# Optimization experiments

Measured on AMD Instinct MI355X. Metric: run time of the kernel, lower is better.

The kernel has to match this reference:

```python
import jax, jax.numpy as jnp
import numpy as np

NEG = -1e30  # log-space 'minus infinity' that stays finite in fp32 arithmetic
BLANK = 0


def _lse3(a, b, c):
    m = jnp.maximum(jnp.maximum(a, b), c)
    return m + jnp.log(jnp.exp(a - m) + jnp.exp(b - m) + jnp.exp(c - m))


def setup_inputs() -> dict:
    key = jax.random.key(0)
    k1, k2, k3, k4 = jax.random.split(key, 4)
    B, T, C, L = 16, 512, 4096, 128
    scores = jax.random.normal(k1, (B, T, C), dtype=jnp.float32)
    labels = jax.random.randint(k2, (B, L), 1, C, dtype=jnp.int64)      # no blanks in targets
    feat_lens = jax.random.randint(k3, (B,), 384, T + 1, dtype=jnp.int64)
    label_lens = jax.random.randint(k4, (B,), 64, L + 1, dtype=jnp.int64)
    return {"scores": scores, "labels": labels, "feat_lens": feat_lens, "label_lens": label_lens}


def reference(scores, labels, feat_lens, label_lens):
    # scores: [B, T, C]. Matches torch: log_softmax then nn.CTCLoss(blank=0,
    # reduction='mean', zero_infinity=True).
    scores = scores.astype(jnp.float32)
    log_probs = jax.nn.log_softmax(scores, axis=-1)                      # [B, T, C]
    B, T, C = scores.shape
    L = labels.shape[1]
    S = 2 * L + 1  # extended label: blank, l1, blank, ..., lL, blank

    ext = jnp.full((B, S), BLANK, dtype=labels.dtype).at[:, 1::2].set(labels)
    # Gather per-(t, extended-symbol) log-probs once: [B, T, S]
    lp = jnp.take_along_axis(log_probs, jnp.broadcast_to(ext[:, None, :], (B, T, S)), axis=2)

    # skip transition s-2 -> s allowed iff ext[s] != blank and ext[s] != ext[s-2]
    skip = jnp.concatenate(
        [jnp.zeros((B, 2), bool), (ext[:, 2:] != ext[:, :-2]) & (ext[:, 2:] != BLANK)], axis=1)

    alpha0 = jnp.full((B, S), NEG, dtype=jnp.float32).at[:, 0].set(lp[:, 0, 0])
    alpha0 = alpha0.at[:, 1].set(jnp.where(label_lens > 0, lp[:, 0, 1], NEG))

    lp_t_first = jnp.swapaxes(lp, 0, 1)  # [T, B, S]

    def step(alpha, xs):
        lp_t, t = xs
        a1 = jnp.pad(alpha, ((0, 0), (1, 0)), constant_values=NEG)[:, :S]
        a2 = jnp.pad(alpha, ((0, 0), (2, 0)), constant_values=NEG)[:, :S]
        a2 = jnp.where(skip, a2, NEG)
        new = lp_t + _lse3(alpha, a1, a2)
        alpha = jnp.where((t < feat_lens)[:, None], new, alpha)  # freeze past feat_len
        return alpha, None

    alpha, _ = jax.lax.scan(step, alpha0, (lp_t_first[1:], jnp.arange(1, T)))

    end = 2 * label_lens  # index of final blank per sample
    a_end = jnp.take_along_axis(alpha, end[:, None], axis=1)[:, 0]
    a_end1 = jnp.where(
        label_lens > 0,
        jnp.take_along_axis(alpha, jnp.maximum(end - 1, 0)[:, None], axis=1)[:, 0], NEG)
    m = jnp.maximum(a_end, a_end1)
    log_lik = m + jnp.log(jnp.exp(a_end - m) + jnp.exp(a_end1 - m))
    loss = -log_lik
    loss = jnp.where(loss > 0.5e30, 0.0, loss)  # zero_infinity=True
    denom = jnp.maximum(label_lens, 1).astype(loss.dtype)
    return jnp.mean(loss / denom)  # torch 'mean': divide by target_lengths, then batch mean
```

## Files before the change

### kernel.cpp

```cpp
#include <hip/hip_runtime.h>

#define T_ 512
#define C_ 4096
#define L_ 128
#define RCPLN2 1.4426950408889634f
#define LN2 0.6931471805599453f
#define NEGL (-1e30f)
#define SCALE_CTR 4.722366482869645e21f
#define SCALE_LOG 72.0f

__device__ __forceinline__ float fexp2(float x) { return __builtin_amdgcn_exp2f(x); }
__device__ __forceinline__ float flog2(float x) { return __builtin_amdgcn_logf(x); }
__device__ __forceinline__ float frcp(float x)  { return __builtin_amdgcn_rcpf(x); }
__device__ __forceinline__ float lg(float x)    { return (x > 0.f) ? flog2(x) : NEGL; }

__global__ __launch_bounds__(256) void k_lse_gather(
    const float* __restrict__ scores, const int* __restrict__ labels,
    const int* __restrict__ feat_lens,
    float* __restrict__ p_lab, float* __restrict__ p_blank) {
  const int row = blockIdx.x;
  const int b = row >> 9;
  const int t = row & (T_ - 1);
  if (t >= feat_lens[b]) return;

  __shared__ float sRow[C_];
  __shared__ float sSum[4];
  const float4* __restrict__ rp4 = (const float4*)(scores + (size_t)row * C_);
  float4* sRow4 = (float4*)sRow;
  const int tid = threadIdx.x;

  float s0 = 0.f, s1 = 0.f, s2 = 0.f, s3 = 0.f;
#pragma unroll
  for (int k = 0; k < 4; ++k) {
    float4 v = rp4[tid + 256 * k];
    sRow4[tid + 256 * k] = v;
    s0 += fexp2(v.x * RCPLN2);
    s1 += fexp2(v.y * RCPLN2);
    s2 += fexp2(v.z * RCPLN2);
    s3 += fexp2(v.w * RCPLN2);
  }
  float s = (s0 + s1) + (s2 + s3);
#pragma unroll
  for (int off = 32; off; off >>= 1) s += __shfl_down(s, off);
  const int wid = tid >> 6, lane = tid & 63;
  if (lane == 0) sSum[wid] = s;
  __syncthreads();
  const float l2sum = flog2((sSum[0] + sSum[1]) + (sSum[2] + sSum[3]));

  if (tid < L_) {
    const int lab = labels[b * L_ + tid];
    p_lab[(size_t)row * L_ + tid] = fexp2(sRow[lab] * RCPLN2 - l2sum);
  } else if (tid == L_) {
    p_blank[row] = fexp2(sRow[0] * RCPLN2 - l2sum);
  }
}

__global__ __launch_bounds__(128) void k_ctc_dp(
    const float* __restrict__ p_lab, const float* __restrict__ p_blank,
    const int* __restrict__ labels, const int* __restrict__ feat_lens,
    const int* __restrict__ label_lens, float* __restrict__ loss_out) {
  const int b = blockIdx.x;
  const int lane = threadIdx.x & 63;
  const int wid = threadIdx.x >> 6;
  const int flen = feat_lens[b];
  const int llen = label_lens[b];
  const int tm = flen >> 1;

  const int l0 = labels[b * L_ + 2 * lane];
  const int l1 = labels[b * L_ + 2 * lane + 1];
  const int lm1 = __shfl_up(l1, 1);
  const int ln0 = __shfl_down(l0, 1);
  const bool skip1 = (lane > 0) && (l0 != lm1);
  const bool skip3 = (l1 != l0);
  const bool skipd = (lane < 63) && (ln0 != l1);

  const float2* __restrict__ llp = (const float2*)(p_lab + (size_t)b * T_ * L_);
  const float* __restrict__ lpl = p_lab + (size_t)b * T_ * L_;
  const float* __restrict__ lbp = p_blank + b * T_;

  __shared__ float sB[257];
  __shared__ float sSb;

  if (wid == 0) {
    const float2 ll0 = llp[lane];
    float a0 = (lane == 0) ? lbp[0] : 0.f;
    float a1 = (lane == 0) ? ll0.x : 0.f;
    float a2 = 0.f, a3 = 0.f, a4 = 0.f;
    float p = 0.f;
    float Sa = 0.f;

    float2 cc[4]; float cb[4];
#pragma unroll
    for (int k = 0; k < 4; ++k) {
      const int tt = min(1 + k, flen - 1);
      cc[k] = llp[tt * 64 + lane]; cb[k] = lbp[tt];
    }
    int t = 1;
    while (t <= tm) {
      float2 nc[4]; float nb[4];
#pragma unroll
      for (int k = 0; k < 4; ++k) {
        const int tt = min(t + 4 + k, flen - 1);
        nc[k] = llp[tt * 64 + lane]; nb[k] = lbp[tt];
      }
#pragma unroll
      for (int k = 0; k < 4; ++k) {
        if (t + k <= tm) {
          const float n3 = cc[k].y * (a3 + a2 + (skip3 ? a1 : 0.f));
          const float n4 = cb[k] * (a4 + a3);
          const float pn = __shfl_up(n3, 1);
          const float n0 = cb[k] * (a0 + p);
          const float n1 = cc[k].x * (a1 + a0 + (skip1 ? p : 0.f));
          const float n2 = cb[k] * (a2 + a1);
          a0 = n0; a1 = n1; a2 = n2; a3 = n3;
          a4 = (lane == 63) ? n4 : 0.f;
          p = (lane == 0) ? 0.f : pn;
        }
        if (k & 1) {
          float m = fmaxf(fmaxf(fmaxf(a0, a1), fmaxf(a2, a3)), a4);
#pragma unroll
          for (int off = 1; off < 64; off <<= 1) m = fmaxf(m, __shfl_xor(m, off));
          const float r = frcp(m) * SCALE_CTR;
          Sa += flog2(m) - SCALE_LOG;
          a0 *= r; a1 *= r; a2 *= r; a3 *= r; a4 *= r; p *= r;
        }
      }
#pragma unroll
      for (int k = 0; k < 4; ++k) { cc[k] = nc[k]; cb[k] = nb[k]; }
      t += 4;
    }
    const float2 cce = llp[tm * 64 + lane];
    const float cbe = lbp[tm];
    const float lb2 = flog2(cbe), lc0 = flog2(cce.x), lc1 = flog2(cce.y);
    const float la0 = lg(a0), la1 = lg(a1), la2 = lg(a2), la3 = lg(a3);
    const float la4 = lg(a4);
    __syncthreads();
    float w0 = la0 + sB[4 * lane + 0] - lb2;
    float w1 = la1 + sB[4 * lane + 1] - lc0;
    float w2 = la2 + sB[4 * lane + 2] - lb2;
    float w3 = la3 + sB[4 * lane + 3] - lc1;
    float m = fmaxf(fmaxf(w0, w1), fmaxf(w2, w3));
    float w4 = NEGL;
    if (lane == 63) { w4 = la4 + sB[256] - lb2; m = fmaxf(m, w4); }
#pragma unroll
    for (int off = 1; off < 64; off <<= 1) m = fmaxf(m, __shfl_xor(m, off));
    float sum = fexp2(w0 - m) + fexp2(w1 - m) + fexp2(w2 - m) + fexp2(w3 - m);
    if (lane == 63) sum += fexp2(w4 - m);
#pragma unroll
    for (int off = 1; off < 64; off <<= 1) sum += __shfl_xor(sum, off);
    if (lane == 0) {
      const float l2lik = m + flog2(sum) + Sa + sSb;
      float loss = -LN2 * l2lik;
      if (loss > 0.5e30f || !(loss == loss)) loss = 0.0f;
      loss_out[b] = loss / (float)llen;
    }
  } else {
    const int e = 2 * llen;
    const float ve = lbp[flen - 1];
    const float vo = lpl[(size_t)(flen - 1) * L_ + (llen - 1)];
    float b0 = (4 * lane == e) ? ve : 0.f;
    float b1 = (4 * lane + 1 == e - 1) ? vo : 0.f;
    float b2 = (4 * lane + 2 == e) ? ve : 0.f;
    float b3 = (4 * lane + 3 == e - 1) ? vo : 0.f;
    float b4 = (lane == 63 && e == 256) ? ve : 0.f;
    float q0 = __shfl_down(b0, 1); q0 = (lane == 63) ? b4 : q0;
    float q1 = __shfl_down(b1, 1); q1 = (lane == 63) ? 0.f : q1;
    float Sb = 0.f;

    float2 cc[4]; float cb[4];
    int t = flen - 2;
#pragma unroll
    for (int k = 0; k < 4; ++k) {
      const int tt = max(t - k, tm);
      cc[k] = llp[tt * 64 + lane]; cb[k] = lbp[tt];
    }
    while (t >= tm) {
      float2 nc[4]; float nb[4];
#pragma unroll
      for (int k = 0; k < 4; ++k) {
        const int tt = max(t - 4 - k, tm);
        nc[k] = llp[tt * 64 + lane]; nb[k] = lbp[tt];
      }
#pragma unroll
      for (int k = 0; k < 4; ++k) {
        if (t - k >= tm) {
          const float n0 = cb[k] * (b0 + b1);
          const float n1 = cc[k].x * (b1 + b2 + (skip3 ? b3 : 0.f));
          const float n4 = cb[k] * b4;
          const float q0n = __shfl_down(n0, 1);
          const float q1n = __shfl_down(n1, 1);
          const float n3 = cc[k].y * (b3 + q0 + (skipd ? q1 : 0.f));
          const float n2 = cb[k] * (b2 + b3);
          b0 = n0; b1 = n1; b2 = n2; b3 = n3; b4 = n4;
          q0 = (lane == 63) ? n4 : q0n;
          q1 = (lane == 63) ? 0.f : q1n;
        }
        if (k & 1) {
          float m = fmaxf(fmaxf(fmaxf(b0, b1), fmaxf(b2, b3)), b4);
#pragma unroll
          for (int off = 1; off < 64; off <<= 1) m = fmaxf(m, __shfl_xor(m, off));
          const float r = frcp(m) * SCALE_CTR;
          Sb += flog2(m) - SCALE_LOG;
          b0 *= r; b1 *= r; b2 *= r; b3 *= r; b4 *= r; q0 *= r; q1 *= r;
        }
      }
#pragma unroll
      for (int k = 0; k < 4; ++k) { cc[k] = nc[k]; cb[k] = nb[k]; }
      t -= 4;
    }
    sB[4 * lane + 0] = lg(b0);
    sB[4 * lane + 1] = lg(b1);
    sB[4 * lane + 2] = lg(b2);
    sB[4 * lane + 3] = lg(b3);
    if (lane == 63) sB[256] = lg(b4);
    if (lane == 0) sSb = Sb;
    __syncthreads();
  }
}

__global__ __launch_bounds__(64) void k_final(const float* __restrict__ loss_out,
                                              float* __restrict__ out, int B) {
  const int tid = threadIdx.x;
  float v = (tid < B) ? loss_out[tid] : 0.0f;
#pragma unroll
  for (int off = 32; off; off >>= 1) v += __shfl_down(v, off);
  if (tid == 0) out[0] = v / (float)B;
}

extern "C" void kernel_launch(void* const* d_in, const int* in_sizes, int n_in,
                              void* d_out, int out_size, void* d_ws, size_t ws_size,
                              hipStream_t stream) {
  const float* scores = (const float*)d_in[0];
  const int* labels = (const int*)d_in[1];
  const int* feat_lens = (const int*)d_in[2];
  const int* label_lens = (const int*)d_in[3];
  const int B = in_sizes[2];

  float* p_lab = (float*)d_ws;
  float* p_blank = p_lab + (size_t)B * T_ * L_;
  float* loss_out = p_blank + (size_t)B * T_;
  float* out = (float*)d_out;

  k_lse_gather<<<B * T_, 256, 0, stream>>>(scores, labels, feat_lens, p_lab, p_blank);
  k_ctc_dp<<<B, 128, 0, stream>>>(p_lab, p_blank, labels, feat_lens, label_lens, loss_out);
  k_final<<<1, 64, 0, stream>>>(loss_out, out, B);
}
```

Before: 243.7 us.

## Use DPP lane shifts and reductions in CTC DP, deepen prefetch

Replaces __shfl_up/__shfl_down/__shfl_xor (LDS-permute based) in the forward and backward CTC recurrences with DPP row/wave shift instructions and a DPP-based wave max reduction. The per-step latency of the serial DP chain is meant to drop. Prefetch depth is doubled to two groups of four timesteps ahead, and the forward loop's midpoint is rounded down to a multiple of four so the per-step bounds check can be removed. The wave_shr/shl DPP controls with bound_ctrl supply zero at the boundary lanes, which replaces the explicit lane-0/lane-63 selects. The approach depends on the DPP wave-shift controls being supported on this architecture.

```diff
diff --git a/kernel.cpp b/kernel.cpp
--- a/kernel.cpp
+++ b/kernel.cpp
@@ -13,6 +13,27 @@
 __device__ __forceinline__ float flog2(float x) { return __builtin_amdgcn_logf(x); }
 __device__ __forceinline__ float frcp(float x)  { return __builtin_amdgcn_rcpf(x); }
 __device__ __forceinline__ float lg(float x)    { return (x > 0.f) ? flog2(x) : NEGL; }
+
+template <int CTRL>
+__device__ __forceinline__ float dppmov(float v) {
+  return __int_as_float(__builtin_amdgcn_update_dpp(
+      0, __float_as_int(v), CTRL, 0xF, 0xF, true));
+}
+__device__ __forceinline__ float wshr1(float v) { return dppmov<0x138>(v); }
+__device__ __forceinline__ float wshl1(float v) { return dppmov<0x130>(v); }
+template <int CTRL>
+__device__ __forceinline__ float maxdpp(float v) {
+  return fmaxf(v, dppmov<CTRL>(v));
+}
+__device__ __forceinline__ float wavemax(float v) {
+  v = maxdpp<0xB1>(v);
+  v = maxdpp<0x4E>(v);
+  v = maxdpp<0x141>(v);
+  v = maxdpp<0x140>(v);
+  v = maxdpp<0x142>(v);
+  v = maxdpp<0x143>(v);
+  return __int_as_float(__builtin_amdgcn_readlane(__float_as_int(v), 63));
+}
 
 __global__ __launch_bounds__(256) void k_lse_gather(
     const float* __restrict__ scores, const int* __restrict__ labels,
@@ -64,7 +85,7 @@
   const int wid = threadIdx.x >> 6;
   const int flen = feat_lens[b];
   const int llen = label_lens[b];
-  const int tm = flen >> 1;
+  const int tm = (flen >> 1) & ~3;
 
   const int l0 = labels[b * L_ + 2 * lane];
   const int l1 = labels[b * L_ + 2 * lane + 1];
@@ -89,44 +110,45 @@
     float p = 0.f;
     float Sa = 0.f;
 
-    float2 cc[4]; float cb[4];
-#pragma unroll
-    for (int k = 0; k < 4; ++k) {
-      const int tt = min(1 + k, flen - 1);
-      cc[k] = llp[tt * 64 + lane]; cb[k] = lbp[tt];
+    float2 cc[4], nc[4]; float cb[4], nb[4];
+#pragma unroll
+    for (int k = 0; k < 4; ++k) {
+      cc[k] = llp[(1 + k) * 64 + lane]; cb[k] = lbp[1 + k];
+    }
+#pragma unroll
+    for (int k = 0; k < 4; ++k) {
+      const int tt = min(5 + k, flen - 1);
+      nc[k] = llp[tt * 64 + lane]; nb[k] = lbp[tt];
     }
     int t = 1;
     while (t <= tm) {
-      float2 nc[4]; float nb[4];
-#pragma unroll
-      for (int k = 0; k < 4; ++k) {
-        const int tt = min(t + 4 + k, flen - 1);
-        nc[k] = llp[tt * 64 + lane]; nb[k] = lbp[tt];
-      }
-#pragma unroll
-      for (int k = 0; k < 4; ++k) {
-        if (t + k <= tm) {
-          const float n3 = cc[k].y * (a3 + a2 + (skip3 ? a1 : 0.f));
-          const float n4 = cb[k] * (a4 + a3);
-          const float pn = __shfl_up(n3, 1);
-          const float n0 = cb[k] * (a0 + p);
-          const float n1 = cc[k].x * (a1 + a0 + (skip1 ? p : 0.f));
-          const float n2 = cb[k] * (a2 + a1);
-          a0 = n0; a1 = n1; a2 = n2; a3 = n3;
-          a4 = (lane == 63) ? n4 : 0.f;
-          p = (lane == 0) ? 0.f : pn;
-        }
+      float2 mc[4]; float mb[4];
+#pragma unroll
+      for (int k = 0; k < 4; ++k) {
+        const int tt = min(t + 8 + k, flen - 1);
+        mc[k] = llp[tt * 64 + lane]; mb[k] = lbp[tt];
+      }
+#pragma unroll
+      for (int k = 0; k < 4; ++k) {
+        const float n3 = cc[k].y * (a3 + a2 + (skip3 ? a1 : 0.f));
+        const float n4 = cb[k] * (a4 + a3);
+        const float pn = wshr1(n3);
+        const float n0 = cb[k] * (a0 + p);
+        const float n1 = cc[k].x * (a1 + a0 + (skip1 ? p : 0.f));
+        const float n2 = cb[k] * (a2 + a1);
+        a0 = n0; a1 = n1; a2 = n2; a3 = n3;
+        a4 = (lane == 63) ? n4 : 0.f;
+        p = pn;
         if (k & 1) {
-          float m = fmaxf(fmaxf(fmaxf(a0, a1), fmaxf(a2, a3)), a4);
-#pragma unroll
-          for (int off = 1; off < 64; off <<= 1) m = fmaxf(m, __shfl_xor(m, off));
+          const float m = wavemax(fmaxf(fmaxf(fmaxf(a0, a1), fmaxf(a2, a3)), a4));
           const float r = frcp(m) * SCALE_CTR;
           Sa += flog2(m) - SCALE_LOG;
           a0 *= r; a1 *= r; a2 *= r; a3 *= r; a4 *= r; p *= r;
         }
       }
 #pragma unroll
-      for (int k = 0; k < 4; ++k) { cc[k] = nc[k]; cb[k] = nb[k]; }
+      for (int k = 0; k < 4; ++k) { cc[k] = nc[k]; cb[k] = nb[k];
+                                    nc[k] = mc[k]; nb[k] = mb[k]; }
       t += 4;
     }
     const float2 cce = llp[tm * 64 + lane];
@@ -167,19 +189,24 @@
     float q1 = __shfl_down(b1, 1); q1 = (lane == 63) ? 0.f : q1;
     float Sb = 0.f;
 
-    float2 cc[4]; float cb[4];
+    float2 cc[4], nc[4]; float cb[4], nb[4];
     int t = flen - 2;
 #pragma unroll
     for (int k = 0; k < 4; ++k) {
       const int tt = max(t - k, tm);
       cc[k] = llp[tt * 64 + lane]; cb[k] = lbp[tt];
     }
+#pragma unroll
+    for (int k = 0; k < 4; ++k) {
+      const int tt = max(t - 4 - k, tm);
+      nc[k] = llp[tt * 64 + lane]; nb[k] = lbp[tt];
+    }
     while (t >= tm) {
-      float2 nc[4]; float nb[4];
-#pragma unroll
-      for (int k = 0; k < 4; ++k) {
-        const int tt = max(t - 4 - k, tm);
-        nc[k] = llp[tt * 64 + lane]; nb[k] = lbp[tt];
+      float2 mc[4]; float mb[4];
+#pragma unroll
+      for (int k = 0; k < 4; ++k) {
+        const int tt = max(t - 8 - k, tm);
+        mc[k] = llp[tt * 64 + lane]; mb[k] = lbp[tt];
       }
 #pragma unroll
       for (int k = 0; k < 4; ++k) {
@@ -187,25 +214,24 @@
           const float n0 = cb[k] * (b0 + b1);
           const float n1 = cc[k].x * (b1 + b2 + (skip3 ? b3 : 0.f));
           const float n4 = cb[k] * b4;
-          const float q0n = __shfl_down(n0, 1);
-          const float q1n = __shfl_down(n1, 1);
+          const float q0n = wshl1(n0);
+          const float q1n = wshl1(n1);
           const float n3 = cc[k].y * (b3 + q0 + (skipd ? q1 : 0.f));
           const float n2 = cb[k] * (b2 + b3);
           b0 = n0; b1 = n1; b2 = n2; b3 = n3; b4 = n4;
           q0 = (lane == 63) ? n4 : q0n;
-          q1 = (lane == 63) ? 0.f : q1n;
+          q1 = q1n;
         }
         if (k & 1) {
-          float m = fmaxf(fmaxf(fmaxf(b0, b1), fmaxf(b2, b3)), b4);
-#pragma unroll
-          for (int off = 1; off < 64; off <<= 1) m = fmaxf(m, __shfl_xor(m, off));
+          const float m = wavemax(fmaxf(fmaxf(fmaxf(b0, b1), fmaxf(b2, b3)), b4));
           const float r = frcp(m) * SCALE_CTR;
           Sb += flog2(m) - SCALE_LOG;
           b0 *= r; b1 *= r; b2 *= r; b3 *= r; b4 *= r; q0 *= r; q1 *= r;
         }
       }
 #pragma unroll
-      for (int k = 0; k < 4; ++k) { cc[k] = nc[k]; cb[k] = nb[k]; }
+      for (int k = 0; k < 4; ++k) { cc[k] = nc[k]; cb[k] = nb[k];
+                                    nc[k] = mc[k]; nb[k] = mb[k]; }
       t -= 4;
     }
     sB[4 * lane + 0] = lg(b0);
```

Result: faster. 222.1 us (-8.9%).

## Speed up CTC DP with DPP shifts, exponent rescaling, deeper prefetch, fused final reduce

Applied to the files above, without the earlier changes.

Lane shifts and the wave max reduction in the alpha/beta recurrences now use DPP row/wave moves instead of ds_bpermute shuffles. Rescaling now works by adjusting the float exponent and keeps an integer scale count, which removes the rcp and log from the serial critical path. Label probabilities are prefetched in four rotating 8-step buffers rather than 4-step ones, and the midpoint is rounded to an even step. The separate final kernel is replaced by an atomic counter where the last block computes the mean, at the cost of an extra memset launch and atomics.

```diff
diff --git a/kernel.cpp b/kernel.cpp
--- a/kernel.cpp
+++ b/kernel.cpp
@@ -6,13 +6,25 @@
 #define RCPLN2 1.4426950408889634f
 #define LN2 0.6931471805599453f
 #define NEGL (-1e30f)
-#define SCALE_CTR 4.722366482869645e21f
-#define SCALE_LOG 72.0f
 
 __device__ __forceinline__ float fexp2(float x) { return __builtin_amdgcn_exp2f(x); }
 __device__ __forceinline__ float flog2(float x) { return __builtin_amdgcn_logf(x); }
-__device__ __forceinline__ float frcp(float x)  { return __builtin_amdgcn_rcpf(x); }
 __device__ __forceinline__ float lg(float x)    { return (x > 0.f) ? flog2(x) : NEGL; }
+
+template <int CTRL>
+__device__ __forceinline__ float dppmov(float v) {
+  return __int_as_float(__builtin_amdgcn_update_dpp(
+      0, __float_as_int(v), CTRL, 0xF, 0xF, true));
+}
+__device__ __forceinline__ float wshr1(float v) { return dppmov<0x138>(v); }
+__device__ __forceinline__ float wshl1(float v) { return dppmov<0x130>(v); }
+template <int CTRL>
+__device__ __forceinline__ float maxdpp(float v) { return fmaxf(v, dppmov<CTRL>(v)); }
+__device__ __forceinline__ float wavemax(float v) {
+  v = maxdpp<0xB1>(v);  v = maxdpp<0x4E>(v);  v = maxdpp<0x141>(v);
+  v = maxdpp<0x140>(v); v = maxdpp<0x142>(v); v = maxdpp<0x143>(v);
+  return __int_as_float(__builtin_amdgcn_readlane(__float_as_int(v), 63));
+}
 
 __global__ __launch_bounds__(256) void k_lse_gather(
     const float* __restrict__ scores, const int* __restrict__ labels,
@@ -55,16 +67,68 @@
   }
 }
 
+#define RESC5(x0,x1,x2,x3,x4,xp,Si) {                                   \
+    const float mm = wavemax(fmaxf(fmaxf(fmaxf(x0,x1),fmaxf(x2,x3)),x4)); \
+    const int Eb = (__float_as_int(mm) >> 23) & 0xFF;                   \
+    const int d = max(Eb - 199, -127);                                  \
+    const float rr = __int_as_float((127 - d) << 23);                   \
+    Si += d;                                                            \
+    x0 *= rr; x1 *= rr; x2 *= rr; x3 *= rr; x4 *= rr; xp *= rr; }
+#define RESC6(x0,x1,x2,x3,x4,xq0,xq1,Si) {                              \
+    const float mm = wavemax(fmaxf(fmaxf(fmaxf(x0,x1),fmaxf(x2,x3)),x4)); \
+    const int Eb = (__float_as_int(mm) >> 23) & 0xFF;                   \
+    const int d = max(Eb - 199, -127);                                  \
+    const float rr = __int_as_float((127 - d) << 23);                   \
+    Si += d;                                                            \
+    x0 *= rr; x1 *= rr; x2 *= rr; x3 *= rr; x4 *= rr; xq0 *= rr; xq1 *= rr; }
+
+#define LOADF(Sc, Sb_, TS) _Pragma("unroll")                            \
+  for (int k = 0; k < 8; ++k) { Sc[k] = llp[(TS + k) * 64 + lane]; Sb_[k] = lbp[TS + k]; }
+#define LOADB(Sc, Sb_, TS) _Pragma("unroll")                            \
+  for (int k = 0; k < 8; ++k) { Sc[k] = llp[(TS - k) * 64 + lane]; Sb_[k] = lbp[TS - k]; }
+
+#define FCHUNK(Sc, Sb_, TS) _Pragma("unroll")                           \
+  for (int k = 0; k < 8; ++k) {                                         \
+    if (TS + k <= tm) {                                                 \
+      const float n3 = Sc[k].y * (a3 + a2 + (skip3 ? a1 : 0.f));        \
+      const float n4 = Sb_[k] * (a4 + a3);                              \
+      const float pn = wshr1(n3);                                       \
+      const float n0 = Sb_[k] * (a0 + p);                               \
+      const float n1 = Sc[k].x * (a1 + a0 + (skip1 ? p : 0.f));         \
+      const float n2 = Sb_[k] * (a2 + a1);                              \
+      a0 = n0; a1 = n1; a2 = n2; a3 = n3;                               \
+      a4 = (lane == 63) ? n4 : 0.f; p = pn;                             \
+    }                                                                   \
+    if (k & 1) RESC5(a0, a1, a2, a3, a4, p, Sa_i)                       \
+  }
+
+#define BCHUNK(Sc, Sb_, TS) _Pragma("unroll")                           \
+  for (int k = 0; k < 8; ++k) {                                         \
+    if (TS - k >= tm) {                                                 \
+      const float n0 = Sb_[k] * (b0 + b1);                              \
+      const float n1 = Sc[k].x * (b1 + b2 + (skip3 ? b3 : 0.f));        \
+      const float n4 = Sb_[k] * b4;                                     \
+      const float q0n = wshl1(n0);                                      \
+      const float q1n = wshl1(n1);                                      \
+      const float n3 = Sc[k].y * (b3 + q0 + (skipd ? q1 : 0.f));        \
+      const float n2 = Sb_[k] * (b2 + b3);                              \
+      b0 = n0; b1 = n1; b2 = n2; b3 = n3; b4 = n4;                      \
+      q0 = (lane == 63) ? n4 : q0n; q1 = q1n;                           \
+    }                                                                   \
+    if (k & 1) RESC6(b0, b1, b2, b3, b4, q0, q1, Sb_i)                  \
+  }
+
 __global__ __launch_bounds__(128) void k_ctc_dp(
     const float* __restrict__ p_lab, const float* __restrict__ p_blank,
     const int* __restrict__ labels, const int* __restrict__ feat_lens,
-    const int* __restrict__ label_lens, float* __restrict__ loss_out) {
+    const int* __restrict__ label_lens, float* __restrict__ loss_out,
+    int* __restrict__ counter, float* __restrict__ out, int B) {
   const int b = blockIdx.x;
   const int lane = threadIdx.x & 63;
   const int wid = threadIdx.x >> 6;
   const int flen = feat_lens[b];
   const int llen = label_lens[b];
-  const int tm = flen >> 1;
+  const int tm = (flen >> 1) & ~1;
 
   const int l0 = labels[b * L_ + 2 * lane];
   const int l1 = labels[b * L_ + 2 * lane + 1];
@@ -79,7 +143,7 @@
   const float* __restrict__ lbp = p_blank + b * T_;
 
   __shared__ float sB[257];
-  __shared__ float sSb;
+  __shared__ int sSbI;
 
   if (wid == 0) {
     const float2 ll0 = llp[lane];
@@ -87,47 +151,18 @@
     float a1 = (lane == 0) ? ll0.x : 0.f;
     float a2 = 0.f, a3 = 0.f, a4 = 0.f;
     float p = 0.f;
-    float Sa = 0.f;
-
-    float2 cc[4]; float cb[4];
-#pragma unroll
-    for (int k = 0; k < 4; ++k) {
-      const int tt = min(1 + k, flen - 1);
-      cc[k] = llp[tt * 64 + lane]; cb[k] = lbp[tt];
-    }
+    int Sa_i = 0;
+
+    float2 Ac[8], Bc[8], Cc[8], Dc[8];
+    float  Ab[8], Bb[8], Cb[8], Db[8];
+    LOADF(Ac, Ab, 1) LOADF(Bc, Bb, 9) LOADF(Cc, Cb, 17)
     int t = 1;
     while (t <= tm) {
-      float2 nc[4]; float nb[4];
-#pragma unroll
-      for (int k = 0; k < 4; ++k) {
-        const int tt = min(t + 4 + k, flen - 1);
-        nc[k] = llp[tt * 64 + lane]; nb[k] = lbp[tt];
-      }
-#pragma unroll
-      for (int k = 0; k < 4; ++k) {
-        if (t + k <= tm) {
-          const float n3 = cc[k].y * (a3 + a2 + (skip3 ? a1 : 0.f));
-          const float n4 = cb[k] * (a4 + a3);
-          const float pn = __shfl_up(n3, 1);
-          const float n0 = cb[k] * (a0 + p);
-          const float n1 = cc[k].x * (a1 + a0 + (skip1 ? p : 0.f));
-          const float n2 = cb[k] * (a2 + a1);
-          a0 = n0; a1 = n1; a2 = n2; a3 = n3;
-          a4 = (lane == 63) ? n4 : 0.f;
-          p = (lane == 0) ? 0.f : pn;
-        }
-        if (k & 1) {
-          float m = fmaxf(fmaxf(fmaxf(a0, a1), fmaxf(a2, a3)), a4);
-#pragma unroll
-          for (int off = 1; off < 64; off <<= 1) m = fmaxf(m, __shfl_xor(m, off));
-          const float r = frcp(m) * SCALE_CTR;
-          Sa += flog2(m) - SCALE_LOG;
-          a0 *= r; a1 *= r; a2 *= r; a3 *= r; a4 *= r; p *= r;
-        }
-      }
-#pragma unroll
-      for (int k = 0; k < 4; ++k) { cc[k] = nc[k]; cb[k] = nb[k]; }
-      t += 4;
+      LOADF(Dc, Db, t + 24) FCHUNK(Ac, Ab, t)
+      LOADF(Ac, Ab, t + 32) FCHUNK(Bc, Bb, t + 8)
+      LOADF(Bc, Bb, t + 40) FCHUNK(Cc, Cb, t + 16)
+      LOADF(Cc, Cb, t + 48) FCHUNK(Dc, Db, t + 24)
+      t += 32;
     }
     const float2 cce = llp[tm * 64 + lane];
     const float cbe = lbp[tm];
@@ -149,10 +184,21 @@
 #pragma unroll
     for (int off = 1; off < 64; off <<= 1) sum += __shfl_xor(sum, off);
     if (lane == 0) {
-      const float l2lik = m + flog2(sum) + Sa + sSb;
+      const float l2lik = m + flog2(sum) + (float)(Sa_i + sSbI);
       float loss = -LN2 * l2lik;
       if (loss > 0.5e30f || !(loss == loss)) loss = 0.0f;
-      loss_out[b] = loss / (float)llen;
+      const float lb = loss / (float)llen;
+      __hip_atomic_store(&loss_out[b], lb, __ATOMIC_RELEASE,
+                         __HIP_MEMORY_SCOPE_AGENT);
+      const int old = __hip_atomic_fetch_add(counter, 1, __ATOMIC_ACQ_REL,
+                                             __HIP_MEMORY_SCOPE_AGENT);
+      if (old == B - 1) {
+        float tot = 0.f;
+        for (int i = 0; i < B; ++i)
+          tot += __hip_atomic_load(&loss_out[i], __ATOMIC_ACQUIRE,
+                                   __HIP_MEMORY_SCOPE_AGENT);
+        out[0] = tot / (float)B;
+      }
     }
   } else {
     const int e = 2 * llen;
@@ -165,66 +211,27 @@
     float b4 = (lane == 63 && e == 256) ? ve : 0.f;
     float q0 = __shfl_down(b0, 1); q0 = (lane == 63) ? b4 : q0;
     float q1 = __shfl_down(b1, 1); q1 = (lane == 63) ? 0.f : q1;
-    float Sb = 0.f;
-
-    float2 cc[4]; float cb[4];
+    int Sb_i = 0;
+
+    float2 Ac[8], Bc[8], Cc[8], Dc[8];
+    float  Ab[8], Bb[8], Cb[8], Db[8];
     int t = flen - 2;
-#pragma unroll
-    for (int k = 0; k < 4; ++k) {
-      const int tt = max(t - k, tm);
-      cc[k] = llp[tt * 64 + lane]; cb[k] = lbp[tt];
-    }
+    LOADB(Ac, Ab, t) LOADB(Bc, Bb, t - 8) LOADB(Cc, Cb, t - 16)
     while (t >= tm) {
-      float2 nc[4]; float nb[4];
-#pragma unroll
-      for (int k = 0; k < 4; ++k) {
-        const int tt = max(t - 4 - k, tm);
-        nc[k] = llp[tt * 64 + lane]; nb[k] = lbp[tt];
-      }
-#pragma unroll
-      for (int k = 0; k < 4; ++k) {
-        if (t - k >= tm) {
-          const float n0 = cb[k] * (b0 + b1);
-          const float n1 = cc[k].x * (b1 + b2 + (skip3 ? b3 : 0.f));
-          const float n4 = cb[k] * b4;
-          const float q0n = __shfl_down(n0, 1);
-          const float q1n = __shfl_down(n1, 1);
-          const float n3 = cc[k].y * (b3 + q0 + (skipd ? q1 : 0.f));
-          const float n2 = cb[k] * (b2 + b3);
-          b0 = n0; b1 = n1; b2 = n2; b3 = n3; b4 = n4;
-          q0 = (lane == 63) ? n4 : q0n;
-          q1 = (lane == 63) ? 0.f : q1n;
-        }
-        if (k & 1) {
-          float m = fmaxf(fmaxf(fmaxf(b0, b1), fmaxf(b2, b3)), b4);
-#pragma unroll
-          for (int off = 1; off < 64; off <<= 1) m = fmaxf(m, __shfl_xor(m, off));
-          const float r = frcp(m) * SCALE_CTR;
-          Sb += flog2(m) - SCALE_LOG;
-          b0 *= r; b1 *= r; b2 *= r; b3 *= r; b4 *= r; q0 *= r; q1 *= r;
-        }
-      }
-#pragma unroll
-      for (int k = 0; k < 4; ++k) { cc[k] = nc[k]; cb[k] = nb[k]; }
-      t -= 4;
+      LOADB(Dc, Db, t - 24) BCHUNK(Ac, Ab, t)
+      LOADB(Ac, Ab, t - 32) BCHUNK(Bc, Bb, t - 8)
+      LOADB(Bc, Bb, t - 40) BCHUNK(Cc, Cb, t - 16)
+      LOADB(Cc, Cb, t - 48) BCHUNK(Dc, Db, t - 24)
+      t -= 32;
     }
     sB[4 * lane + 0] = lg(b0);
     sB[4 * lane + 1] = lg(b1);
     sB[4 * lane + 2] = lg(b2);
     sB[4 * lane + 3] = lg(b3);
     if (lane == 63) sB[256] = lg(b4);
-    if (lane == 0) sSb = Sb;
+    if (lane == 0) sSbI = Sb_i;
     __syncthreads();
   }
-}
-
-__global__ __launch_bounds__(64) void k_final(const float* __restrict__ loss_out,
-                                              float* __restrict__ out, int B) {
-  const int tid = threadIdx.x;
-  float v = (tid < B) ? loss_out[tid] : 0.0f;
-#pragma unroll
-  for (int off = 32; off; off >>= 1) v += __shfl_down(v, off);
-  if (tid == 0) out[0] = v / (float)B;
 }
 
 extern "C" void kernel_launch(void* const* d_in, const int* in_sizes, int n_in,
@@ -239,9 +246,11 @@
   float* p_lab = (float*)d_ws;
   float* p_blank = p_lab + (size_t)B * T_ * L_;
   float* loss_out = p_blank + (size_t)B * T_;
+  int* counter = (int*)(loss_out + B);
   float* out = (float*)d_out;
 
+  hipMemsetAsync(counter, 0, sizeof(int), stream);
   k_lse_gather<<<B * T_, 256, 0, stream>>>(scores, labels, feat_lens, p_lab, p_blank);
-  k_ctc_dp<<<B, 128, 0, stream>>>(p_lab, p_blank, labels, feat_lens, label_lens, loss_out);
-  k_final<<<1, 64, 0, stream>>>(loss_out, out, B);
-}
+  k_ctc_dp<<<B, 128, 0, stream>>>(p_lab, p_blank, labels, feat_lens, label_lens,
+                                  loss_out, counter, out, B);
+}
```

New measurement: 223.6 us. -8.2%, faster.
